# Performance work log

Measured on AMD Instinct MI355X. Metric: run time of the kernel, lower is better.

Reference implementation:

```python
import jax, jax.numpy as jnp
import numpy as np

B, N, C, H = 8, 512, 64, 128
T, K = 10, 2                       # dilation threshold and skip divisor
TAUS = (0.25, 0.5, 0.75)
WTS = (0.25, 0.5, 0.25)
EPS_GIN = 0.0                      # (1 + eps) * x, eps buffer
AVG_DEG = 32.0


def setup_inputs() -> dict:
    key = jax.random.key(0)
    ks = jax.random.split(key, 6)
    x = jax.random.normal(ks[0], (B, N, C), jnp.float32)
    u = jax.random.uniform(ks[1], (B, N, N))
    a = u < (AVG_DEG / N)
    adj = jnp.maximum(a, jnp.swapaxes(a, 1, 2)).astype(jnp.float32)  # symmetric binary adjacency
    mask = jax.random.bernoulli(ks[2], 0.9, (B, N))
    W1 = jax.random.normal(ks[3], (C, H), jnp.float32) / np.float32(np.sqrt(C))
    b1 = jnp.zeros((H,), jnp.float32)
    W2 = jax.random.normal(ks[4], (H, C), jnp.float32) / np.float32(np.sqrt(H))
    b2 = jnp.zeros((C,), jnp.float32)
    return {"x": x, "adj": adj, "mask": mask, "W1": W1, "b1": b1, "W2": W2, "b2": b2}


def reference(x, adj, mask, W1, b1, W2, b2):
    Bc, Nc, Cc = x.shape
    eye = jnp.eye(Nc, dtype=bool)
    adj_ = jnp.where(eye, 1.0, adj)                 # add_loop=True: force self loops
    # ---- vectorized dilation (replaces the per-(b,n) python loop) ----
    neigh = (adj_ > 0) & (~eye)                     # neighbors excluding self [B,N,N]
    ni = neigh.astype(jnp.int32)
    rank = jnp.cumsum(ni, axis=-1) - ni             # exclusive rank of m among n's sorted neighbors
    nb = ni.sum(-1)                                 # [B,N] neighbor count (w/o self)
    skip = jnp.where(nb > T, (nb + K - 1) // K, 1)  # ceil(nb/k) if nb > T else 1 (linear mode, layer 1)
    skip = jnp.maximum(skip, 1)
    sk = skip[:, :, None]
    # remove relative indices skip-1, 2*skip-1, ... when skip > 1, only for masked-in nodes
    rem = neigh & (sk > 1) & ((rank % sk) == (sk - 1)) & mask[:, :, None]
    rem = rem | jnp.swapaxes(rem, 1, 2)             # symmetric removal
    adj_d = jnp.where(rem, 0.0, adj_)
    # ---- masked quantile aggregation over neighbors (== nanquantile) ----
    nd = adj_d > 0                                  # includes self loop -> at least 1 valid
    vals = jnp.where(nd[..., None], x[:, None, :, :], jnp.inf)  # [B,N,M,C]; invalid -> +inf
    s = jnp.sort(vals, axis=2)                      # valid values first, ascending
    nv = nd.sum(2)                                  # [B,N] valid count per node
    agg = jnp.zeros_like(x)
    for tau, w in zip(TAUS, WTS):                   # small fixed loop over quantiles
        pos = jnp.asarray(tau, x.dtype) * jnp.maximum(nv - 1, 0).astype(x.dtype)
        lo = jnp.floor(pos).astype(jnp.int32)
        hi = jnp.ceil(pos).astype(jnp.int32)
        frac = (pos - lo.astype(x.dtype))[..., None]
        idx_lo = jnp.broadcast_to(lo[:, :, None, None], (Bc, Nc, 1, Cc))
        idx_hi = jnp.broadcast_to(hi[:, :, None, None], (Bc, Nc, 1, Cc))
        v_lo = jnp.take_along_axis(s, idx_lo, axis=2)[:, :, 0, :]
        v_hi = jnp.take_along_axis(s, idx_hi, axis=2)[:, :, 0, :]
        agg = agg + jnp.asarray(w, x.dtype) * (v_lo + frac * (v_hi - v_lo))
    agg = jnp.where(nv[..., None] > 0, agg, 0.0)    # nan_to_num for empty rows
    out = (1.0 + EPS_GIN) * x + agg
    h = jax.nn.relu(out @ W1 + b1)                  # GIN MLP: Linear-ReLU-Linear
    y = h @ W2 + b2
    return y * mask[..., None].astype(y.dtype)
```

## Files before the change

### kernel.cpp

```cpp
#include <hip/hip_runtime.h>
#include <cstdint>

#define B_ 8
#define N_ 512
#define C_ 64
#define H_ 128
#define T_ 10
#define K_ 2
#define WPR 16
#define NVMAX 96
#define TT 8
#define RINV_ROWS (NVMAX + 8)

__device__ inline uint32_t fkey(float v) {
    uint32_t bits = __float_as_uint(v);
    return (bits & 0x80000000u) ? ~bits : (bits | 0x80000000u);
}
__device__ inline float fdec(uint32_t key) {
    uint32_t ok = (key & 0xFFFFFF00u) | 0x80u;
    uint32_t bits = (ok & 0x80000000u) ? (ok ^ 0x80000000u) : ~ok;
    return __uint_as_float(bits);
}

__global__ __launch_bounds__(256) void pass1_keep(const float* __restrict__ adj,
                                                  const int* __restrict__ mask,
                                                  uint32_t* __restrict__ keepbits,
                                                  uint32_t* __restrict__ remT) {
    int wid = threadIdx.x >> 6, lane = threadIdx.x & 63;
    int row = blockIdx.x * 4 + wid;
    int bb = row >> 9;
    int i = row & (N_ - 1);
    const float4* arow4 = (const float4*)(adj + (size_t)row * N_);
    float4 a0 = arow4[lane * 2];
    float4 a1 = arow4[lane * 2 + 1];
    float av[8] = {a0.x, a0.y, a0.z, a0.w, a1.x, a1.y, a1.z, a1.w};

    int flags = 0, cnt = 0;
    int jbase = lane * 8;
#pragma unroll
    for (int k = 0; k < 8; ++k) {
        int j = jbase + k;
        bool ng = (j != i) && (av[k] > 0.0f);
        flags |= ((int)ng) << k;
        cnt += (int)ng;
    }
    int inc = cnt;
#pragma unroll
    for (int d = 1; d < 64; d <<= 1) {
        int o = __shfl_up(inc, d, 64);
        if (lane >= d) inc += o;
    }
    int excl = inc - cnt;
    int nb = __shfl(inc, 63, 64);
    int skip = (nb > T_) ? ((nb + K_ - 1) / K_) : 1;
    if (skip < 1) skip = 1;
    int maski = mask[row];

    unsigned remb = 0;
    if (skip > 1 && maski != 0) {
        int r = excl;
#pragma unroll
        for (int k = 0; k < 8; ++k) {
            if ((flags >> k) & 1) {
                if (r % skip == skip - 1) remb |= 1u << k;
                ++r;
            }
        }
    }
    unsigned diagb = (i >= jbase && i < jbase + 8) ? (1u << (i - jbase)) : 0u;
    unsigned keepb = (((unsigned)flags | diagb) & ~remb) & 0xFFu;

    unsigned rb = remb;
    while (rb) {
        int k = __ffs(rb) - 1; rb &= rb - 1;
        int j = jbase + k;
        atomicOr(&remT[(size_t)(bb * N_ + j) * WPR + (i >> 5)], 1u << (i & 31));
    }

    unsigned p0 = __shfl((int)keepb, (lane & 15) * 4 + 0, 64);
    unsigned p1 = __shfl((int)keepb, (lane & 15) * 4 + 1, 64);
    unsigned p2 = __shfl((int)keepb, (lane & 15) * 4 + 2, 64);
    unsigned p3 = __shfl((int)keepb, (lane & 15) * 4 + 3, 64);
    if (lane < WPR) {
        uint32_t w = (p0 & 0xFFu) | ((p1 & 0xFFu) << 8) |
                     ((p2 & 0xFFu) << 16) | ((p3 & 0xFFu) << 24);
        keepbits[(size_t)row * WPR + lane] = w;
    }
}

__global__ __launch_bounds__(512, 8) void pass2_quant_mlp(
        const float* __restrict__ x,
        const int* __restrict__ mask, const uint32_t* __restrict__ keepbits,
        const uint32_t* __restrict__ remT,
        const float* __restrict__ W1, const float* __restrict__ b1,
        const float* __restrict__ W2, const float* __restrict__ b2,
        float* __restrict__ out) {
    int row = blockIdx.x;
    int b = row >> 9, i = row & (N_ - 1);
    int tid = threadIdx.x;
    int lane = tid & 63;
    int q = tid >> 6;

    __shared__ unsigned short kept[NVMAX];
    __shared__ int s_cnt;
    __shared__ uint32_t keys[NVMAX * C_];
    __shared__ float selv[6 * C_];
    __shared__ unsigned char rankinv[RINV_ROWS * C_];
    float* mlp_buf = (float*)keys;

    if (tid == 0) s_cnt = 0;
    __syncthreads();

    const float* xb = x + (size_t)b * N_ * C_;
    float xself = 0.0f; int mv = 0;
    if (tid < C_) {
        xself = xb[(size_t)i * C_ + tid];
        mv = mask[row];
    }

    {
        int j = tid;
        uint32_t w = keepbits[(size_t)row * WPR + (j >> 5)]
                   & ~remT[(size_t)row * WPR + (j >> 5)];
        bool keep = (w >> (j & 31)) & 1u;
        unsigned long long bal = __ballot(keep);
        int base = 0;
        if (lane == 0 && bal) base = atomicAdd(&s_cnt, __popcll(bal));
        base = __shfl(base, 0, 64);
        if (keep) {
            int pos = __popcll(bal & ((1ull << lane) - 1ull));
            int p = base + pos;
            if (p < NVMAX) kept[p] = (unsigned short)j;
        }
    }
    __syncthreads();
    int nv = s_cnt;
    if (nv > NVMAX) nv = NVMAX;

    for (int t = q; t < nv; t += 8) {
        float v = xb[(size_t)kept[t] * C_ + lane];
        keys[t * C_ + lane] = (fkey(v) & 0xFFFFFF00u) | (uint32_t)t;
    }
    __syncthreads();

    const uint32_t* kcol = keys + lane;

    for (int base = 0; base < nv; base += 64) {
        int tbase = base + q * TT;
        if (tbase >= nv) continue;
        uint32_t k[TT];
        int ra[TT], rb[TT];
#pragma unroll
        for (int m = 0; m < TT; ++m) {
            int t = tbase + m;
            k[m] = (t < nv) ? kcol[t * C_] : 0xFFFFFFFFu;
            ra[m] = 0; rb[m] = 0;
        }
        int u = 0;
#pragma unroll 2
        for (; u + 3 < nv; u += 4) {
            uint32_t w0 = kcol[u * C_];
            uint32_t w1v = kcol[(u + 1) * C_];
            uint32_t w2 = kcol[(u + 2) * C_];
            uint32_t w3 = kcol[(u + 3) * C_];
#pragma unroll
            for (int m = 0; m < TT; ++m) {
                ra[m] += (int)(w0 < k[m]);
                rb[m] += (int)(w1v < k[m]);
                ra[m] += (int)(w2 < k[m]);
                rb[m] += (int)(w3 < k[m]);
            }
        }
        for (; u < nv; ++u) {
            uint32_t w0 = kcol[u * C_];
#pragma unroll
            for (int m = 0; m < TT; ++m) ra[m] += (int)(w0 < k[m]);
        }
#pragma unroll
        for (int m = 0; m < TT; ++m) {
            int rs = ra[m] + rb[m];
            rankinv[rs * C_ + lane] = (unsigned char)(tbase + m);
        }
    }
    __syncthreads();

    if (tid < 6 * C_) {
        int qq = tid >> 6, ch = tid & 63;
        const float taus[3] = {0.25f, 0.5f, 0.75f};
        float nm1 = (float)((nv - 1 > 0) ? nv - 1 : 0);
        float pos = taus[qq >> 1] * nm1;
        int r = (qq & 1) ? (int)ceilf(pos) : (int)floorf(pos);
        int t = rankinv[r * C_ + ch];
        selv[qq * C_ + ch] = fdec(keys[t * C_ + ch]);
    }
    __syncthreads();

    if (tid < C_) {
        float nm1 = (float)((nv - 1 > 0) ? nv - 1 : 0);
        float p0 = 0.25f * nm1, p1 = 0.5f * nm1, p2 = 0.75f * nm1;
        float f0 = p0 - floorf(p0), f1 = p1 - floorf(p1), f2 = p2 - floorf(p2);
        float agg = 0.25f * (selv[0 * C_ + tid] + f0 * (selv[1 * C_ + tid] - selv[0 * C_ + tid]));
        agg      += 0.5f  * (selv[2 * C_ + tid] + f1 * (selv[3 * C_ + tid] - selv[2 * C_ + tid]));
        agg      += 0.25f * (selv[4 * C_ + tid] + f2 * (selv[5 * C_ + tid] - selv[4 * C_ + tid]));
        mlp_buf[tid] = xself + agg;
    }
    __syncthreads();

    {
        int hcol = tid & 127, cq = tid >> 7;
        float acc = 0.0f;
#pragma unroll 4
        for (int c = 0; c < 16; ++c) {
            int c0 = cq * 16 + c;
            acc += mlp_buf[c0] * W1[c0 * H_ + hcol];
        }
        mlp_buf[192 + tid] = acc;
    }
    __syncthreads();
    if (tid < H_) {
        float h = b1[tid] + mlp_buf[192 + tid] + mlp_buf[320 + tid]
                + mlp_buf[448 + tid] + mlp_buf[576 + tid];
        mlp_buf[64 + tid] = h > 0.0f ? h : 0.0f;
    }
    __syncthreads();

    {
        int ycol = tid & 63, kq = tid >> 6;
        float acc = 0.0f;
#pragma unroll 4
        for (int kk = 0; kk < 16; ++kk) {
            int k0 = kq * 16 + kk;
            acc += mlp_buf[64 + k0] * W2[k0 * C_ + ycol];
        }
        mlp_buf[192 + tid] = acc;
    }
    __syncthreads();
    if (tid < C_) {
        float maskf = (mv != 0) ? 1.0f : 0.0f;
        float y = b2[tid];
#pragma unroll
        for (int e = 0; e < 8; ++e) y += mlp_buf[192 + tid + 64 * e];
        out[(size_t)row * C_ + tid] = y * maskf;
    }
}

extern "C" void kernel_launch(void* const* d_in, const int* in_sizes, int n_in,
                              void* d_out, int out_size, void* d_ws, size_t ws_size,
                              hipStream_t stream) {
    const float* x   = (const float*)d_in[0];
    const float* adj = (const float*)d_in[1];
    const int*  mask = (const int*)d_in[2];
    const float* W1  = (const float*)d_in[3];
    const float* b1  = (const float*)d_in[4];
    const float* W2  = (const float*)d_in[5];
    const float* b2  = (const float*)d_in[6];
    float* out = (float*)d_out;

    uint32_t* keepbits = (uint32_t*)d_ws;
    uint32_t* remT     = keepbits + (size_t)B_ * N_ * WPR;

    hipMemsetAsync(remT, 0, (size_t)B_ * N_ * WPR * sizeof(uint32_t), stream);
    hipLaunchKernelGGL(pass1_keep, dim3(B_ * N_ / 4), dim3(256), 0, stream,
                       adj, mask, keepbits, remT);
    hipLaunchKernelGGL(pass2_quant_mlp, dim3(B_ * N_), dim3(512), 0, stream,
                       x, mask, keepbits, remT, W1, b1, W2, b2, out);
}
```

Baseline: 157.8 us.

## Fuse dilation and quantile-MLP passes into one persistent kernel with grid barrier

Merges the two kernels into one launch. Each block first computes the dilation keep/remove bits for 4 rows, then waits at a software grid-wide barrier built on an atomic counter. After the barrier it processes the same 4 rows through the quantile ranking and the MLP in a loop. This removes a kernel launch and the gap between passes, but it needs all 1024 blocks to be resident at once to avoid deadlock, and each block now handles its 4 rows serially.

```diff
diff --git a/kernel.cpp b/kernel.cpp
--- a/kernel.cpp
+++ b/kernel.cpp
@@ -11,6 +11,8 @@
 #define NVMAX 96
 #define TT 8
 #define RINV_ROWS (NVMAX + 8)
+#define RPB 4
+#define NBLK (B_ * N_ / RPB)
 
 __device__ inline uint32_t fkey(float v) {
     uint32_t bits = __float_as_uint(v);
@@ -22,81 +24,25 @@
     return __uint_as_float(bits);
 }
 
-__global__ __launch_bounds__(256) void pass1_keep(const float* __restrict__ adj,
-                                                  const int* __restrict__ mask,
-                                                  uint32_t* __restrict__ keepbits,
-                                                  uint32_t* __restrict__ remT) {
-    int wid = threadIdx.x >> 6, lane = threadIdx.x & 63;
-    int row = blockIdx.x * 4 + wid;
-    int bb = row >> 9;
-    int i = row & (N_ - 1);
-    const float4* arow4 = (const float4*)(adj + (size_t)row * N_);
-    float4 a0 = arow4[lane * 2];
-    float4 a1 = arow4[lane * 2 + 1];
-    float av[8] = {a0.x, a0.y, a0.z, a0.w, a1.x, a1.y, a1.z, a1.w};
-
-    int flags = 0, cnt = 0;
-    int jbase = lane * 8;
-#pragma unroll
-    for (int k = 0; k < 8; ++k) {
-        int j = jbase + k;
-        bool ng = (j != i) && (av[k] > 0.0f);
-        flags |= ((int)ng) << k;
-        cnt += (int)ng;
+__device__ inline void grid_barrier(uint32_t* cnt, int tid) {
+    __syncthreads();
+    if (tid == 0) {
+        __threadfence();
+        atomicAdd(cnt, 1u);
+        while (atomicAdd(cnt, 0u) < (uint32_t)NBLK) __builtin_amdgcn_s_sleep(8);
+        __threadfence();
     }
-    int inc = cnt;
-#pragma unroll
-    for (int d = 1; d < 64; d <<= 1) {
-        int o = __shfl_up(inc, d, 64);
-        if (lane >= d) inc += o;
-    }
-    int excl = inc - cnt;
-    int nb = __shfl(inc, 63, 64);
-    int skip = (nb > T_) ? ((nb + K_ - 1) / K_) : 1;
-    if (skip < 1) skip = 1;
-    int maski = mask[row];
-
-    unsigned remb = 0;
-    if (skip > 1 && maski != 0) {
-        int r = excl;
-#pragma unroll
-        for (int k = 0; k < 8; ++k) {
-            if ((flags >> k) & 1) {
-                if (r % skip == skip - 1) remb |= 1u << k;
-                ++r;
-            }
-        }
-    }
-    unsigned diagb = (i >= jbase && i < jbase + 8) ? (1u << (i - jbase)) : 0u;
-    unsigned keepb = (((unsigned)flags | diagb) & ~remb) & 0xFFu;
-
-    unsigned rb = remb;
-    while (rb) {
-        int k = __ffs(rb) - 1; rb &= rb - 1;
-        int j = jbase + k;
-        atomicOr(&remT[(size_t)(bb * N_ + j) * WPR + (i >> 5)], 1u << (i & 31));
-    }
-
-    unsigned p0 = __shfl((int)keepb, (lane & 15) * 4 + 0, 64);
-    unsigned p1 = __shfl((int)keepb, (lane & 15) * 4 + 1, 64);
-    unsigned p2 = __shfl((int)keepb, (lane & 15) * 4 + 2, 64);
-    unsigned p3 = __shfl((int)keepb, (lane & 15) * 4 + 3, 64);
-    if (lane < WPR) {
-        uint32_t w = (p0 & 0xFFu) | ((p1 & 0xFFu) << 8) |
-                     ((p2 & 0xFFu) << 16) | ((p3 & 0xFFu) << 24);
-        keepbits[(size_t)row * WPR + lane] = w;
-    }
-}
-
-__global__ __launch_bounds__(512, 8) void pass2_quant_mlp(
-        const float* __restrict__ x,
-        const int* __restrict__ mask, const uint32_t* __restrict__ keepbits,
-        const uint32_t* __restrict__ remT,
+    __syncthreads();
+}
+
+__global__ __launch_bounds__(512, 8) void fused_gin(
+        const float* __restrict__ x, const float* __restrict__ adj,
+        const int* __restrict__ mask,
         const float* __restrict__ W1, const float* __restrict__ b1,
         const float* __restrict__ W2, const float* __restrict__ b2,
-        float* __restrict__ out) {
-    int row = blockIdx.x;
-    int b = row >> 9, i = row & (N_ - 1);
+        float* __restrict__ out,
+        uint32_t* __restrict__ keepbits, uint32_t* __restrict__ remT,
+        uint32_t* __restrict__ barcnt) {
     int tid = threadIdx.x;
     int lane = tid & 63;
     int q = tid >> 6;
@@ -108,139 +54,208 @@
     __shared__ unsigned char rankinv[RINV_ROWS * C_];
     float* mlp_buf = (float*)keys;
 
-    if (tid == 0) s_cnt = 0;
-    __syncthreads();
-
-    const float* xb = x + (size_t)b * N_ * C_;
-    float xself = 0.0f; int mv = 0;
-    if (tid < C_) {
-        xself = xb[(size_t)i * C_ + tid];
-        mv = mask[row];
+    if (q < RPB) {
+        int row = blockIdx.x * RPB + q;
+        int bb = row >> 9;
+        int i = row & (N_ - 1);
+        const float4* arow4 = (const float4*)(adj + (size_t)row * N_);
+        float4 a0 = arow4[lane * 2];
+        float4 a1 = arow4[lane * 2 + 1];
+        float av[8] = {a0.x, a0.y, a0.z, a0.w, a1.x, a1.y, a1.z, a1.w};
+
+        int flags = 0, cnt = 0;
+        int jbase = lane * 8;
+#pragma unroll
+        for (int k = 0; k < 8; ++k) {
+            int j = jbase + k;
+            bool ng = (j != i) && (av[k] > 0.0f);
+            flags |= ((int)ng) << k;
+            cnt += (int)ng;
+        }
+        int inc = cnt;
+#pragma unroll
+        for (int d = 1; d < 64; d <<= 1) {
+            int o = __shfl_up(inc, d, 64);
+            if (lane >= d) inc += o;
+        }
+        int excl = inc - cnt;
+        int nb = __shfl(inc, 63, 64);
+        int skip = (nb > T_) ? ((nb + K_ - 1) / K_) : 1;
+        if (skip < 1) skip = 1;
+        int maski = mask[row];
+
+        unsigned remb = 0;
+        if (skip > 1 && maski != 0) {
+            int r = excl;
+#pragma unroll
+            for (int k = 0; k < 8; ++k) {
+                if ((flags >> k) & 1) {
+                    if (r % skip == skip - 1) remb |= 1u << k;
+                    ++r;
+                }
+            }
+        }
+        unsigned diagb = (i >= jbase && i < jbase + 8) ? (1u << (i - jbase)) : 0u;
+        unsigned keepb = (((unsigned)flags | diagb) & ~remb) & 0xFFu;
+
+        unsigned rb = remb;
+        while (rb) {
+            int k = __ffs(rb) - 1; rb &= rb - 1;
+            int j = jbase + k;
+            atomicOr(&remT[(size_t)(bb * N_ + j) * WPR + (i >> 5)], 1u << (i & 31));
+        }
+
+        unsigned p0 = __shfl((int)keepb, (lane & 15) * 4 + 0, 64);
+        unsigned p1 = __shfl((int)keepb, (lane & 15) * 4 + 1, 64);
+        unsigned p2 = __shfl((int)keepb, (lane & 15) * 4 + 2, 64);
+        unsigned p3 = __shfl((int)keepb, (lane & 15) * 4 + 3, 64);
+        if (lane < WPR) {
+            uint32_t w = (p0 & 0xFFu) | ((p1 & 0xFFu) << 8) |
+                         ((p2 & 0xFFu) << 16) | ((p3 & 0xFFu) << 24);
+            keepbits[(size_t)row * WPR + lane] = w;
+        }
     }
-
-    {
-        int j = tid;
-        uint32_t w = keepbits[(size_t)row * WPR + (j >> 5)]
-                   & ~remT[(size_t)row * WPR + (j >> 5)];
-        bool keep = (w >> (j & 31)) & 1u;
-        unsigned long long bal = __ballot(keep);
-        int base = 0;
-        if (lane == 0 && bal) base = atomicAdd(&s_cnt, __popcll(bal));
-        base = __shfl(base, 0, 64);
-        if (keep) {
-            int pos = __popcll(bal & ((1ull << lane) - 1ull));
-            int p = base + pos;
-            if (p < NVMAX) kept[p] = (unsigned short)j;
-        }
-    }
-    __syncthreads();
-    int nv = s_cnt;
-    if (nv > NVMAX) nv = NVMAX;
-
-    for (int t = q; t < nv; t += 8) {
-        float v = xb[(size_t)kept[t] * C_ + lane];
-        keys[t * C_ + lane] = (fkey(v) & 0xFFFFFF00u) | (uint32_t)t;
-    }
-    __syncthreads();
-
-    const uint32_t* kcol = keys + lane;
-
-    for (int base = 0; base < nv; base += 64) {
-        int tbase = base + q * TT;
-        if (tbase >= nv) continue;
-        uint32_t k[TT];
-        int ra[TT], rb[TT];
-#pragma unroll
-        for (int m = 0; m < TT; ++m) {
-            int t = tbase + m;
-            k[m] = (t < nv) ? kcol[t * C_] : 0xFFFFFFFFu;
-            ra[m] = 0; rb[m] = 0;
-        }
-        int u = 0;
+    grid_barrier(barcnt, tid);
+
+    for (int r = 0; r < RPB; ++r) {
+        int row = blockIdx.x * RPB + r;
+        int b = row >> 9, i = row & (N_ - 1);
+
+        __syncthreads();
+        if (tid == 0) s_cnt = 0;
+        __syncthreads();
+
+        const float* xb = x + (size_t)b * N_ * C_;
+        float xself = 0.0f; int mv = 0;
+        if (tid < C_) {
+            xself = xb[(size_t)i * C_ + tid];
+            mv = mask[row];
+        }
+
+        {
+            int j = tid;
+            uint32_t w = keepbits[(size_t)row * WPR + (j >> 5)]
+                       & ~remT[(size_t)row * WPR + (j >> 5)];
+            bool keep = (w >> (j & 31)) & 1u;
+            unsigned long long bal = __ballot(keep);
+            int base = 0;
+            if (lane == 0 && bal) base = atomicAdd(&s_cnt, __popcll(bal));
+            base = __shfl(base, 0, 64);
+            if (keep) {
+                int pos = __popcll(bal & ((1ull << lane) - 1ull));
+                int p = base + pos;
+                if (p < NVMAX) kept[p] = (unsigned short)j;
+            }
+        }
+        __syncthreads();
+        int nv = s_cnt;
+        if (nv > NVMAX) nv = NVMAX;
+
+        for (int t = q; t < nv; t += 8) {
+            float v = xb[(size_t)kept[t] * C_ + lane];
+            keys[t * C_ + lane] = (fkey(v) & 0xFFFFFF00u) | (uint32_t)t;
+        }
+        __syncthreads();
+
+        const uint32_t* kcol = keys + lane;
+
+        for (int base = 0; base < nv; base += 64) {
+            int tbase = base + q * TT;
+            if (tbase >= nv) continue;
+            uint32_t k[TT];
+            int ra[TT], rb[TT];
+#pragma unroll
+            for (int m = 0; m < TT; ++m) {
+                int t = tbase + m;
+                k[m] = (t < nv) ? kcol[t * C_] : 0xFFFFFFFFu;
+                ra[m] = 0; rb[m] = 0;
+            }
+            int u = 0;
 #pragma unroll 2
-        for (; u + 3 < nv; u += 4) {
-            uint32_t w0 = kcol[u * C_];
-            uint32_t w1v = kcol[(u + 1) * C_];
-            uint32_t w2 = kcol[(u + 2) * C_];
-            uint32_t w3 = kcol[(u + 3) * C_];
+            for (; u + 3 < nv; u += 4) {
+                uint32_t w0 = kcol[u * C_];
+                uint32_t w1v = kcol[(u + 1) * C_];
+                uint32_t w2 = kcol[(u + 2) * C_];
+                uint32_t w3 = kcol[(u + 3) * C_];
+#pragma unroll
+                for (int m = 0; m < TT; ++m) {
+                    ra[m] += (int)(w0 < k[m]);
+                    rb[m] += (int)(w1v < k[m]);
+                    ra[m] += (int)(w2 < k[m]);
+                    rb[m] += (int)(w3 < k[m]);
+                }
+            }
+            for (; u < nv; ++u) {
+                uint32_t w0 = kcol[u * C_];
+#pragma unroll
+                for (int m = 0; m < TT; ++m) ra[m] += (int)(w0 < k[m]);
+            }
 #pragma unroll
             for (int m = 0; m < TT; ++m) {
-                ra[m] += (int)(w0 < k[m]);
-                rb[m] += (int)(w1v < k[m]);
-                ra[m] += (int)(w2 < k[m]);
-                rb[m] += (int)(w3 < k[m]);
-            }
-        }
-        for (; u < nv; ++u) {
-            uint32_t w0 = kcol[u * C_];
-#pragma unroll
-            for (int m = 0; m < TT; ++m) ra[m] += (int)(w0 < k[m]);
-        }
-#pragma unroll
-        for (int m = 0; m < TT; ++m) {
-            int rs = ra[m] + rb[m];
-            rankinv[rs * C_ + lane] = (unsigned char)(tbase + m);
-        }
-    }
-    __syncthreads();
-
-    if (tid < 6 * C_) {
-        int qq = tid >> 6, ch = tid & 63;
-        const float taus[3] = {0.25f, 0.5f, 0.75f};
-        float nm1 = (float)((nv - 1 > 0) ? nv - 1 : 0);
-        float pos = taus[qq >> 1] * nm1;
-        int r = (qq & 1) ? (int)ceilf(pos) : (int)floorf(pos);
-        int t = rankinv[r * C_ + ch];
-        selv[qq * C_ + ch] = fdec(keys[t * C_ + ch]);
-    }
-    __syncthreads();
-
-    if (tid < C_) {
-        float nm1 = (float)((nv - 1 > 0) ? nv - 1 : 0);
-        float p0 = 0.25f * nm1, p1 = 0.5f * nm1, p2 = 0.75f * nm1;
-        float f0 = p0 - floorf(p0), f1 = p1 - floorf(p1), f2 = p2 - floorf(p2);
-        float agg = 0.25f * (selv[0 * C_ + tid] + f0 * (selv[1 * C_ + tid] - selv[0 * C_ + tid]));
-        agg      += 0.5f  * (selv[2 * C_ + tid] + f1 * (selv[3 * C_ + tid] - selv[2 * C_ + tid]));
-        agg      += 0.25f * (selv[4 * C_ + tid] + f2 * (selv[5 * C_ + tid] - selv[4 * C_ + tid]));
-        mlp_buf[tid] = xself + agg;
-    }
-    __syncthreads();
-
-    {
-        int hcol = tid & 127, cq = tid >> 7;
-        float acc = 0.0f;
+                int rs = ra[m] + rb[m];
+                rankinv[rs * C_ + lane] = (unsigned char)(tbase + m);
+            }
+        }
+        __syncthreads();
+
+        if (tid < 6 * C_) {
+            int qq = tid >> 6, ch = tid & 63;
+            const float taus[3] = {0.25f, 0.5f, 0.75f};
+            float nm1 = (float)((nv - 1 > 0) ? nv - 1 : 0);
+            float pos = taus[qq >> 1] * nm1;
+            int rr = (qq & 1) ? (int)ceilf(pos) : (int)floorf(pos);
+            int t = rankinv[rr * C_ + ch];
+            selv[qq * C_ + ch] = fdec(keys[t * C_ + ch]);
+        }
+        __syncthreads();
+
+        if (tid < C_) {
+            float nm1 = (float)((nv - 1 > 0) ? nv - 1 : 0);
+            float p0 = 0.25f * nm1, p1 = 0.5f * nm1, p2 = 0.75f * nm1;
+            float f0 = p0 - floorf(p0), f1 = p1 - floorf(p1), f2 = p2 - floorf(p2);
+            float agg = 0.25f * (selv[0 * C_ + tid] + f0 * (selv[1 * C_ + tid] - selv[0 * C_ + tid]));
+            agg      += 0.5f  * (selv[2 * C_ + tid] + f1 * (selv[3 * C_ + tid] - selv[2 * C_ + tid]));
+            agg      += 0.25f * (selv[4 * C_ + tid] + f2 * (selv[5 * C_ + tid] - selv[4 * C_ + tid]));
+            mlp_buf[tid] = xself + agg;
+        }
+        __syncthreads();
+
+        {
+            int hcol = tid & 127, cq = tid >> 7;
+            float acc = 0.0f;
 #pragma unroll 4
-        for (int c = 0; c < 16; ++c) {
-            int c0 = cq * 16 + c;
-            acc += mlp_buf[c0] * W1[c0 * H_ + hcol];
-        }
-        mlp_buf[192 + tid] = acc;
-    }
-    __syncthreads();
-    if (tid < H_) {
-        float h = b1[tid] + mlp_buf[192 + tid] + mlp_buf[320 + tid]
-                + mlp_buf[448 + tid] + mlp_buf[576 + tid];
-        mlp_buf[64 + tid] = h > 0.0f ? h : 0.0f;
-    }
-    __syncthreads();
-
-    {
-        int ycol = tid & 63, kq = tid >> 6;
-        float acc = 0.0f;
+            for (int c = 0; c < 16; ++c) {
+                int c0 = cq * 16 + c;
+                acc += mlp_buf[c0] * W1[c0 * H_ + hcol];
+            }
+            mlp_buf[192 + tid] = acc;
+        }
+        __syncthreads();
+        if (tid < H_) {
+            float h = b1[tid] + mlp_buf[192 + tid] + mlp_buf[320 + tid]
+                    + mlp_buf[448 + tid] + mlp_buf[576 + tid];
+            mlp_buf[64 + tid] = h > 0.0f ? h : 0.0f;
+        }
+        __syncthreads();
+
+        {
+            int ycol = tid & 63, kq = tid >> 6;
+            float acc = 0.0f;
 #pragma unroll 4
-        for (int kk = 0; kk < 16; ++kk) {
-            int k0 = kq * 16 + kk;
-            acc += mlp_buf[64 + k0] * W2[k0 * C_ + ycol];
-        }
-        mlp_buf[192 + tid] = acc;
-    }
-    __syncthreads();
-    if (tid < C_) {
-        float maskf = (mv != 0) ? 1.0f : 0.0f;
-        float y = b2[tid];
-#pragma unroll
-        for (int e = 0; e < 8; ++e) y += mlp_buf[192 + tid + 64 * e];
-        out[(size_t)row * C_ + tid] = y * maskf;
+            for (int kk = 0; kk < 16; ++kk) {
+                int k0 = kq * 16 + kk;
+                acc += mlp_buf[64 + k0] * W2[k0 * C_ + ycol];
+            }
+            mlp_buf[192 + tid] = acc;
+        }
+        __syncthreads();
+        if (tid < C_) {
+            float maskf = (mv != 0) ? 1.0f : 0.0f;
+            float y = b2[tid];
+#pragma unroll
+            for (int e = 0; e < 8; ++e) y += mlp_buf[192 + tid + 64 * e];
+            out[(size_t)row * C_ + tid] = y * maskf;
+        }
     }
 }
 
@@ -256,12 +271,12 @@
     const float* b2  = (const float*)d_in[6];
     float* out = (float*)d_out;
 
-    uint32_t* keepbits = (uint32_t*)d_ws;
-    uint32_t* remT     = keepbits + (size_t)B_ * N_ * WPR;
-
-    hipMemsetAsync(remT, 0, (size_t)B_ * N_ * WPR * sizeof(uint32_t), stream);
-    hipLaunchKernelGGL(pass1_keep, dim3(B_ * N_ / 4), dim3(256), 0, stream,
-                       adj, mask, keepbits, remT);
-    hipLaunchKernelGGL(pass2_quant_mlp, dim3(B_ * N_), dim3(512), 0, stream,
-                       x, mask, keepbits, remT, W1, b1, W2, b2, out);
-}
+    uint32_t* remT     = (uint32_t*)d_ws;
+    uint32_t* barcnt   = remT + (size_t)B_ * N_ * WPR;
+    uint32_t* keepbits = barcnt + 64;
+
+    hipMemsetAsync(remT, 0, (size_t)B_ * N_ * WPR * sizeof(uint32_t) + 256, stream);
+    hipLaunchKernelGGL(fused_gin, dim3(NBLK), dim3(512), 0, stream,
+                       x, adj, mask, W1, b1, W2, b2, out,
+                       keepbits, remT, barcnt);
+}
```

After: 255.9 us. 1.62x slower.
